# Kernel optimization log

Hardware: AMD Instinct MI355X
Metric: run time of the kernel (lower is better)

## Reference

```python
import jax, jax.numpy as jnp
import numpy as np

NHEAD = 16

def setup_inputs() -> dict:
    key = jax.random.key(0)
    ks = jax.random.split(key, 7)
    b, l, d = 4, 2048, 1024
    s = 1.0 / np.sqrt(d)
    return {
        "Q": jax.random.normal(ks[0], (b, l, d), jnp.float32),
        "K": jax.random.normal(ks[1], (b, l, d), jnp.float32),
        "V": jax.random.normal(ks[2], (b, l, d), jnp.float32),
        "WQ": jax.random.normal(ks[3], (d, d), jnp.float32) * s,
        "WK": jax.random.normal(ks[4], (d, d), jnp.float32) * s,
        "WV": jax.random.normal(ks[5], (d, d), jnp.float32) * s,
        "WO": jax.random.normal(ks[6], (d, d), jnp.float32) * s,
    }

def reference(Q, K, V, WQ, WK, WV, WO):
    # WQ/WK/WV/WO stored torch-style as [out, in]; Linear(x) = x @ W.T
    b, lq, d = Q.shape
    lk = K.shape[1]
    h = NHEAD
    dk = d // h
    # project and split heads: [b, l, h, dk]
    q = (Q @ WQ.T).reshape(b, lq, h, dk)
    k = (K @ WK.T).reshape(b, lk, h, dk)
    v = (V @ WV.T).reshape(b, lk, h, dk)
    # scaled dot-product attention (dropout = identity in eval mode)
    scale = 1.0 / jnp.sqrt(jnp.asarray(dk, Q.dtype))
    score = jnp.einsum('bqhd,bkhd->bhqk', q, k) * scale  # [b,h,lq,lk]
    attn = jax.nn.softmax(score, axis=-1)
    o = jnp.einsum('bhqk,bkhd->bqhd', attn, v).reshape(b, lq, h * dk)
    return o @ WO.T
```

## Files before the change

kernel.cpp:

```cpp
#include <hip/hip_runtime.h>
#include <stdint.h>

#define D_MODEL 1024
#define NHEADS 16
#define DKH 64
#define SEQ 2048
#define BATCH 4
#define M_TOT (BATCH * SEQ)
#define LOG2E 1.44269504088896340736f

typedef __bf16 v8bf __attribute__((ext_vector_type(8)));
typedef __bf16 v4bf __attribute__((ext_vector_type(4)));
typedef _Float16 v8h __attribute__((ext_vector_type(8)));
typedef _Float16 v4h __attribute__((ext_vector_type(4)));
typedef float v4f __attribute__((ext_vector_type(4)));

typedef const __attribute__((address_space(1))) void* gas_ptr;
typedef __attribute__((address_space(3))) void* las_ptr;

static __device__ __forceinline__ void async16(const void* g, void* l) {
    __builtin_amdgcn_global_load_lds((gas_ptr)g, (las_ptr)l, 16, 0, 0);
}

static __device__ __forceinline__ v4f mfma16x32(v8bf a, v8bf b, v4f c) {
    return __builtin_amdgcn_mfma_f32_16x16x32_bf16(a, b, c, 0, 0, 0);
}
static __device__ __forceinline__ v4f mfma16x16h(v4h a, v4h b, v4f c) {
    return __builtin_amdgcn_mfma_f32_16x16x16f16(a, b, c, 0, 0, 0);
}

__global__ __launch_bounds__(256) void cvt_x(const float* __restrict__ src,
                                             __bf16* __restrict__ dst) {
    int i = blockIdx.x * 256 + threadIdx.x;
    const float4* s = (const float4*)src;
    float4 a = s[2 * i], b = s[2 * i + 1];
    v8bf o;
    o[0] = (__bf16)a.x; o[1] = (__bf16)a.y; o[2] = (__bf16)a.z; o[3] = (__bf16)a.w;
    o[4] = (__bf16)b.x; o[5] = (__bf16)b.y; o[6] = (__bf16)b.z; o[7] = (__bf16)b.w;
    *(v8bf*)(dst + (size_t)i * 8) = o;
}

__global__ __launch_bounds__(256) void cvt_w(const float* __restrict__ w0,
                                             const float* __restrict__ w1,
                                             const float* __restrict__ w2,
                                             const float* __restrict__ w3,
                                             __bf16* __restrict__ dst) {
    int gid = blockIdx.x * 256 + threadIdx.x;
    int tsel = gid >> 17;
    int off = gid & 131071;
    const float* s = (tsel == 0) ? w0 : (tsel == 1) ? w1 : (tsel == 2) ? w2 : w3;
    const float4* sp = (const float4*)s + 2 * (size_t)off;
    float4 a = sp[0], b = sp[1];
    v8bf o;
    o[0] = (__bf16)a.x; o[1] = (__bf16)a.y; o[2] = (__bf16)a.z; o[3] = (__bf16)a.w;
    o[4] = (__bf16)b.x; o[5] = (__bf16)b.y; o[6] = (__bf16)b.z; o[7] = (__bf16)b.w;
    *(v8bf*)(dst + ((size_t)tsel << 20) + (size_t)off * 8) = o;
}

template <int LAYOUT>
__global__ __launch_bounds__(256) void gemm_nt(const __bf16* __restrict__ A,
                                               const __bf16* __restrict__ W,
                                               void* __restrict__ Cv, float scale) {
    const int t = threadIdx.x, lane = t & 63, wave = t >> 6;
    const int r = lane & 15, qd = lane >> 4;
    const int m0 = blockIdx.x * 128, n0 = blockIdx.y * 128;
    const int mw = (wave & 1) * 64, nw = (wave >> 1) * 64;

    __shared__ __align__(16) __bf16 As[128 * 32];
    __shared__ __align__(16) __bf16 Bs[128 * 32];

    const int wc = (lane & 3) ^ ((lane >> 3) & 3);
    const int wrow = lane >> 2;
    const int rdpos = (qd ^ ((r >> 1) & 3)) * 8;

    v4f acc[4][4] = {};
    for (int k0 = 0; k0 < D_MODEL; k0 += 32) {
#pragma unroll
        for (int p = 0; p < 2; ++p) {
            int rb = (p * 4 + wave) * 16;
            async16(A + (size_t)(m0 + rb + wrow) * D_MODEL + k0 + wc * 8, &As[rb * 32]);
            async16(W + (size_t)(n0 + rb + wrow) * D_MODEL + k0 + wc * 8, &Bs[rb * 32]);
        }
        __syncthreads();
        v8bf af[4], bfr[4];
#pragma unroll
        for (int mt = 0; mt < 4; ++mt)
            af[mt] = *(const v8bf*)&As[(mw + mt * 16 + r) * 32 + rdpos];
#pragma unroll
        for (int nt = 0; nt < 4; ++nt)
            bfr[nt] = *(const v8bf*)&Bs[(nw + nt * 16 + r) * 32 + rdpos];
#pragma unroll
        for (int mt = 0; mt < 4; ++mt)
#pragma unroll
            for (int nt = 0; nt < 4; ++nt)
                acc[mt][nt] = mfma16x32(af[mt], bfr[nt], acc[mt][nt]);
        __syncthreads();
    }

#pragma unroll
    for (int mt = 0; mt < 4; ++mt)
#pragma unroll
        for (int nt = 0; nt < 4; ++nt) {
            int row = m0 + mw + mt * 16 + qd * 4;
            int col = n0 + nw + nt * 16 + r;
            if (LAYOUT == 0) {
                float* C = (float*)Cv;
#pragma unroll
                for (int i = 0; i < 4; ++i)
                    C[(size_t)(row + i) * D_MODEL + col] = acc[mt][nt][i];
            } else {
                int bb = row >> 11, l = row & (SEQ - 1);
                int h = col >> 6, d = col & (DKH - 1);
                if (LAYOUT == 2) {
                    int pos = (l & ~31) + (((l >> 2) & 3) << 3) + (((l >> 4) & 1) << 2);
                    _Float16* vt = (_Float16*)Cv;
                    v4h o;
#pragma unroll
                    for (int i = 0; i < 4; ++i) o[i] = (_Float16)acc[mt][nt][i];
                    *(v4h*)&vt[((size_t)((bb * NHEADS + h) * DKH + d)) * SEQ + pos] = o;
                } else {
                    __bf16* dst = (__bf16*)Cv;
#pragma unroll
                    for (int i = 0; i < 4; ++i)
                        dst[(((size_t)(bb * NHEADS + h) * SEQ) + l + i) * DKH + d] =
                            (__bf16)(acc[mt][nt][i] * scale);
                }
            }
        }
}

__global__ __launch_bounds__(256, 2) void attn_kernel(const __bf16* __restrict__ qh,
                                                      const __bf16* __restrict__ kh,
                                                      const _Float16* __restrict__ vt,
                                                      __bf16* __restrict__ oh) {
    const int lane = threadIdx.x & 63, wave = threadIdx.x >> 6;
    const int r = lane & 15, qd = lane >> 4;
    const int id = blockIdx.x;
    const int bh = (id & 7) * 8 + ((id >> 3) & 7);
    const int q0 = (id >> 6) * 256 + wave * 64;

    __shared__ __align__(16) __bf16 Kb[2][64 * 64];
    __shared__ __align__(16) _Float16 Vb[2][64 * 64];

    const __bf16* kbh = kh + (size_t)bh * SEQ * DKH;
    const _Float16* vbh = vt + (size_t)bh * DKH * SEQ;

    v8bf qf[4][2];
#pragma unroll
    for (int a = 0; a < 4; ++a) {
        const __bf16* qp = qh + ((size_t)bh * SEQ + q0 + a * 16 + r) * DKH + qd * 8;
        qf[a][0] = *(const v8bf*)qp;
        qf[a][1] = *(const v8bf*)(qp + 32);
    }

    v4f oacc[4][4] = {};
    v4f psum[4] = {};
    v4h ones;
    ones[0] = (_Float16)1.f; ones[1] = (_Float16)1.f;
    ones[2] = (_Float16)1.f; ones[3] = (_Float16)1.f;

    const int srow = lane >> 3;
    const int sc = (lane & 7) ^ srow;
    const int rs = r & 7;

#pragma unroll
    for (int p = 0; p < 2; ++p) {
        int rb = wave * 16 + p * 8;
        async16(kbh + (size_t)(rb + srow) * DKH + sc * 8, &Kb[0][rb * 64]);
        async16(vbh + (size_t)(rb + srow) * SEQ + sc * 8, &Vb[0][rb * 64]);
    }

    for (int tt = 0; tt < SEQ / 64; ++tt) {
        const int buf = tt & 1;
        __syncthreads();
        if (tt + 1 < SEQ / 64) {
            const int t0 = (tt + 1) * 64;
#pragma unroll
            for (int p = 0; p < 2; ++p) {
                int rb = wave * 16 + p * 8;
                async16(kbh + (size_t)(t0 + rb + srow) * DKH + sc * 8, &Kb[buf ^ 1][rb * 64]);
                async16(vbh + (size_t)(rb + srow) * SEQ + t0 + sc * 8, &Vb[buf ^ 1][rb * 64]);
            }
        }
        const __bf16* Kc = Kb[buf];
        const _Float16* Vc = Vb[buf];
#pragma unroll
        for (int kb = 0; kb < 2; ++kb) {
            v4h pf[2][4];
#pragma unroll
            for (int kg = 0; kg < 2; ++kg) {
                int row = kb * 32 + kg * 16 + r;
                v8bf ka = *(const v8bf*)&Kc[row * 64 + (qd ^ rs) * 8];
                v8bf kc = *(const v8bf*)&Kc[row * 64 + ((qd + 4) ^ rs) * 8];
#pragma unroll
                for (int a = 0; a < 4; ++a) {
                    v4f s = mfma16x32(ka, qf[a][0], v4f{});
                    s = mfma16x32(kc, qf[a][1], s);
#pragma unroll
                    for (int i = 0; i < 4; ++i)
                        pf[kg][a][i] = (_Float16)__builtin_exp2f(s[i]);
                }
            }
#pragma unroll
            for (int a = 0; a < 4; ++a) {
                psum[a] = mfma16x16h(ones, pf[0][a], psum[a]);
                psum[a] = mfma16x16h(ones, pf[1][a], psum[a]);
            }
#pragma unroll
            for (int g = 0; g < 4; ++g) {
                v8h vv = *(const v8h*)&Vc[(g * 16 + r) * 64 + ((kb * 4 + qd) ^ rs) * 8];
                v4h vlo = __builtin_shufflevector(vv, vv, 0, 1, 2, 3);
                v4h vhi = __builtin_shufflevector(vv, vv, 4, 5, 6, 7);
#pragma unroll
                for (int a = 0; a < 4; ++a) {
                    oacc[a][g] = mfma16x16h(vlo, pf[0][a], oacc[a][g]);
                    oacc[a][g] = mfma16x16h(vhi, pf[1][a], oacc[a][g]);
                }
            }
        }
    }

    const int b = bh >> 4, h = bh & (NHEADS - 1);
#pragma unroll
    for (int a = 0; a < 4; ++a) {
        float inv = 1.0f / psum[a][0];
        int l = q0 + a * 16 + r;
        __bf16* op = oh + (((size_t)(b * SEQ + l)) * NHEADS + h) * DKH + qd * 4;
#pragma unroll
        for (int g = 0; g < 4; ++g) {
            v4bf ov;
#pragma unroll
            for (int i = 0; i < 4; ++i) ov[i] = (__bf16)(oacc[a][g][i] * inv);
            *(v4bf*)(op + g * 16) = ov;
        }
    }
}

extern "C" void kernel_launch(void* const* d_in, const int* in_sizes, int n_in,
                              void* d_out, int out_size, void* d_ws, size_t ws_size,
                              hipStream_t stream) {
    const float* Q = (const float*)d_in[0];
    const float* K = (const float*)d_in[1];
    const float* V = (const float*)d_in[2];
    const float* WQ = (const float*)d_in[3];
    const float* WK = (const float*)d_in[4];
    const float* WV = (const float*)d_in[5];
    const float* WO = (const float*)d_in[6];
    float* out = (float*)d_out;

    const size_t elems = (size_t)M_TOT * D_MODEL;
    const size_t welems = (size_t)D_MODEL * D_MODEL;
    __bf16* wb = (__bf16*)d_ws;
    __bf16* xb = wb + 4 * welems;
    __bf16* qh = xb + elems;
    __bf16* kh = qh + elems;
    _Float16* vtb = (_Float16*)(kh + elems);
    __bf16* oh = (__bf16*)(vtb + elems);

    dim3 gg(M_TOT / 128, D_MODEL / 128);

    cvt_w<<<2048, 256, 0, stream>>>(WQ, WK, WV, WO, wb);
    cvt_x<<<4096, 256, 0, stream>>>(Q, xb);
    gemm_nt<1><<<gg, 256, 0, stream>>>(xb, wb, qh, 0.125f * LOG2E);
    cvt_x<<<4096, 256, 0, stream>>>(K, xb);
    gemm_nt<1><<<gg, 256, 0, stream>>>(xb, wb + welems, kh, 1.0f);
    cvt_x<<<4096, 256, 0, stream>>>(V, xb);
    gemm_nt<2><<<gg, 256, 0, stream>>>(xb, wb + 2 * welems, vtb, 1.0f);
    attn_kernel<<<512, 256, 0, stream>>>(qh, kh, vtb, oh);
    gemm_nt<0><<<gg, 256, 0, stream>>>(oh, wb + 3 * welems, out, 1.0f);
}
```

Baseline: 371.0 us.

## Switch attention inner loop to 32x32x16 MFMA with permlane-swapped P fragments

Rewrites the attention kernel to use 32x32x16 bf16/f16 MFMA tiles instead of 16x16 tiles for both QK^T and PV. The exp'd scores are packed to f16 with cvt_pkrtz and rearranged across half-waves with permlane32_swap so they can feed the PV MFMA directly. The V-transpose store drops its interleaved position permutation. The row sum is now accumulated with VALU adds and a cross-lane shuffle instead of an MFMA against a ones vector. The aim is fewer MFMA issues and fewer LDS fragment loads per tile, at the cost of more register pressure from the 16-wide accumulators and extra permute instructions.

```diff
diff --git a/kernel.cpp b/kernel.cpp
--- a/kernel.cpp
+++ b/kernel.cpp
@@ -14,6 +14,9 @@
 typedef _Float16 v8h __attribute__((ext_vector_type(8)));
 typedef _Float16 v4h __attribute__((ext_vector_type(4)));
 typedef float v4f __attribute__((ext_vector_type(4)));
+typedef float v16f __attribute__((ext_vector_type(16)));
+typedef unsigned int v4u __attribute__((ext_vector_type(4)));
+typedef unsigned int v2u __attribute__((ext_vector_type(2)));
 
 typedef const __attribute__((address_space(1))) void* gas_ptr;
 typedef __attribute__((address_space(3))) void* las_ptr;
@@ -25,8 +28,19 @@
 static __device__ __forceinline__ v4f mfma16x32(v8bf a, v8bf b, v4f c) {
     return __builtin_amdgcn_mfma_f32_16x16x32_bf16(a, b, c, 0, 0, 0);
 }
-static __device__ __forceinline__ v4f mfma16x16h(v4h a, v4h b, v4f c) {
-    return __builtin_amdgcn_mfma_f32_16x16x16f16(a, b, c, 0, 0, 0);
+static __device__ __forceinline__ v16f mfma32x16bf(v8bf a, v8bf b, v16f c) {
+    return __builtin_amdgcn_mfma_f32_32x32x16_bf16(a, b, c, 0, 0, 0);
+}
+static __device__ __forceinline__ v16f mfma32x16h(v8h a, v8h b, v16f c) {
+    return __builtin_amdgcn_mfma_f32_32x32x16_f16(a, b, c, 0, 0, 0);
+}
+static __device__ __forceinline__ unsigned pkh(float a, float b) {
+    return __builtin_bit_cast(unsigned, __builtin_amdgcn_cvt_pkrtz(a, b));
+}
+static __device__ __forceinline__ void plswap(unsigned& x, unsigned& y) {
+    v2u r = __builtin_amdgcn_permlane32_swap(x, y, false, false);
+    x = r[0];
+    y = r[1];
 }
 
 __global__ __launch_bounds__(256) void cvt_x(const float* __restrict__ src,
@@ -112,12 +126,11 @@
                 int bb = row >> 11, l = row & (SEQ - 1);
                 int h = col >> 6, d = col & (DKH - 1);
                 if (LAYOUT == 2) {
-                    int pos = (l & ~31) + (((l >> 2) & 3) << 3) + (((l >> 4) & 1) << 2);
                     _Float16* vt = (_Float16*)Cv;
                     v4h o;
 #pragma unroll
                     for (int i = 0; i < 4; ++i) o[i] = (_Float16)acc[mt][nt][i];
-                    *(v4h*)&vt[((size_t)((bb * NHEADS + h) * DKH + d)) * SEQ + pos] = o;
+                    *(v4h*)&vt[((size_t)((bb * NHEADS + h) * DKH + d)) * SEQ + l] = o;
                 } else {
                     __bf16* dst = (__bf16*)Cv;
 #pragma unroll
@@ -134,7 +147,7 @@
                                                       const _Float16* __restrict__ vt,
                                                       __bf16* __restrict__ oh) {
     const int lane = threadIdx.x & 63, wave = threadIdx.x >> 6;
-    const int r = lane & 15, qd = lane >> 4;
+    const int l31 = lane & 31, hi = lane >> 5, l7 = lane & 7;
     const int id = blockIdx.x;
     const int bh = (id & 7) * 8 + ((id >> 3) & 7);
     const int q0 = (id >> 6) * 256 + wave * 64;
@@ -145,23 +158,19 @@
     const __bf16* kbh = kh + (size_t)bh * SEQ * DKH;
     const _Float16* vbh = vt + (size_t)bh * DKH * SEQ;
 
-    v8bf qf[4][2];
-#pragma unroll
-    for (int a = 0; a < 4; ++a) {
-        const __bf16* qp = qh + ((size_t)bh * SEQ + q0 + a * 16 + r) * DKH + qd * 8;
-        qf[a][0] = *(const v8bf*)qp;
-        qf[a][1] = *(const v8bf*)(qp + 32);
-    }
-
-    v4f oacc[4][4] = {};
-    v4f psum[4] = {};
-    v4h ones;
-    ones[0] = (_Float16)1.f; ones[1] = (_Float16)1.f;
-    ones[2] = (_Float16)1.f; ones[3] = (_Float16)1.f;
+    v8bf qf[2][4];
+#pragma unroll
+    for (int qa = 0; qa < 2; ++qa)
+#pragma unroll
+        for (int c = 0; c < 4; ++c)
+            qf[qa][c] = *(const v8bf*)&qh[((size_t)bh * SEQ + q0 + qa * 32 + l31) * DKH +
+                                          c * 16 + hi * 8];
+
+    v16f oacc[2][2] = {};
+    float ps[2] = {0.f, 0.f};
 
     const int srow = lane >> 3;
     const int sc = (lane & 7) ^ srow;
-    const int rs = r & 7;
 
 #pragma unroll
     for (int p = 0; p < 2; ++p) {
@@ -186,53 +195,62 @@
         const _Float16* Vc = Vb[buf];
 #pragma unroll
         for (int kb = 0; kb < 2; ++kb) {
-            v4h pf[2][4];
-#pragma unroll
-            for (int kg = 0; kg < 2; ++kg) {
-                int row = kb * 32 + kg * 16 + r;
-                v8bf ka = *(const v8bf*)&Kc[row * 64 + (qd ^ rs) * 8];
-                v8bf kc = *(const v8bf*)&Kc[row * 64 + ((qd + 4) ^ rs) * 8];
-#pragma unroll
-                for (int a = 0; a < 4; ++a) {
-                    v4f s = mfma16x32(ka, qf[a][0], v4f{});
-                    s = mfma16x32(kc, qf[a][1], s);
-#pragma unroll
-                    for (int i = 0; i < 4; ++i)
-                        pf[kg][a][i] = (_Float16)__builtin_exp2f(s[i]);
+            v8bf ka[4];
+#pragma unroll
+            for (int c = 0; c < 4; ++c)
+                ka[c] = *(const v8bf*)&Kc[(kb * 32 + l31) * 64 + (((c * 2 + hi) ^ l7) << 3)];
+            v8h pb[2][2];
+#pragma unroll
+            for (int qa = 0; qa < 2; ++qa) {
+                v16f d = {};
+#pragma unroll
+                for (int c = 0; c < 4; ++c) d = mfma32x16bf(ka[c], qf[qa][c], d);
+                float e[16];
+#pragma unroll
+                for (int i = 0; i < 16; ++i) e[i] = __builtin_exp2f(d[i]);
+                ps[qa] += (((e[0] + e[1]) + (e[2] + e[3])) + ((e[4] + e[5]) + (e[6] + e[7]))) +
+                          (((e[8] + e[9]) + (e[10] + e[11])) + ((e[12] + e[13]) + (e[14] + e[15])));
+#pragma unroll
+                for (int kc = 0; kc < 2; ++kc) {
+                    unsigned a0 = pkh(e[kc * 8 + 0], e[kc * 8 + 1]);
+                    unsigned a1 = pkh(e[kc * 8 + 2], e[kc * 8 + 3]);
+                    unsigned b0 = pkh(e[kc * 8 + 4], e[kc * 8 + 5]);
+                    unsigned b1 = pkh(e[kc * 8 + 6], e[kc * 8 + 7]);
+                    plswap(a0, b0);
+                    plswap(a1, b1);
+                    v4u w = {a0, a1, b0, b1};
+                    pb[qa][kc] = __builtin_bit_cast(v8h, w);
                 }
             }
 #pragma unroll
-            for (int a = 0; a < 4; ++a) {
-                psum[a] = mfma16x16h(ones, pf[0][a], psum[a]);
-                psum[a] = mfma16x16h(ones, pf[1][a], psum[a]);
-            }
+            for (int dg = 0; dg < 2; ++dg)
+#pragma unroll
+                for (int kc = 0; kc < 2; ++kc) {
+                    v8h va = *(const v8h*)&Vc[(dg * 32 + l31) * 64 +
+                                              (((kb * 4 + kc * 2 + hi) ^ l7) << 3)];
+#pragma unroll
+                    for (int qa = 0; qa < 2; ++qa)
+                        oacc[qa][dg] = mfma32x16h(va, pb[qa][kc], oacc[qa][dg]);
+                }
+        }
+    }
+
+    const int b = bh >> 4, h = bh & (NHEADS - 1);
+#pragma unroll
+    for (int qa = 0; qa < 2; ++qa) {
+        float tot = ps[qa] + __shfl_xor(ps[qa], 32, 64);
+        float inv = 1.0f / tot;
+        int lq = q0 + qa * 32 + l31;
+        __bf16* op = oh + (((size_t)(b * SEQ + lq)) * NHEADS + h) * DKH;
+#pragma unroll
+        for (int dg = 0; dg < 2; ++dg)
 #pragma unroll
             for (int g = 0; g < 4; ++g) {
-                v8h vv = *(const v8h*)&Vc[(g * 16 + r) * 64 + ((kb * 4 + qd) ^ rs) * 8];
-                v4h vlo = __builtin_shufflevector(vv, vv, 0, 1, 2, 3);
-                v4h vhi = __builtin_shufflevector(vv, vv, 4, 5, 6, 7);
-#pragma unroll
-                for (int a = 0; a < 4; ++a) {
-                    oacc[a][g] = mfma16x16h(vlo, pf[0][a], oacc[a][g]);
-                    oacc[a][g] = mfma16x16h(vhi, pf[1][a], oacc[a][g]);
-                }
-            }
-        }
-    }
-
-    const int b = bh >> 4, h = bh & (NHEADS - 1);
-#pragma unroll
-    for (int a = 0; a < 4; ++a) {
-        float inv = 1.0f / psum[a][0];
-        int l = q0 + a * 16 + r;
-        __bf16* op = oh + (((size_t)(b * SEQ + l)) * NHEADS + h) * DKH + qd * 4;
-#pragma unroll
-        for (int g = 0; g < 4; ++g) {
-            v4bf ov;
-#pragma unroll
-            for (int i = 0; i < 4; ++i) ov[i] = (__bf16)(oacc[a][g][i] * inv);
-            *(v4bf*)(op + g * 16) = ov;
-        }
+                v4bf ov;
+#pragma unroll
+                for (int i = 0; i < 4; ++i) ov[i] = (__bf16)(oacc[qa][dg][g * 4 + i] * inv);
+                *(v4bf*)(op + dg * 32 + g * 8 + hi * 4) = ov;
+            }
     }
 }
 
```

New measurement: 369.4 us. No clear change (-0.4%).
